# Kernel optimization log

Hardware: AMD Instinct MI355X
Metric: run time of the kernel (lower is better)

The kernel has to match this reference:

```python
import jax, jax.numpy as jnp
import numpy as np


def setup_inputs() -> dict:
    key = jax.random.key(0)
    k1, k2 = jax.random.split(key)
    B, Tc, Tq, D = 8, 2048, 1024, 1024
    similarity = jax.random.normal(k1, (B, Tc, Tq), dtype=jnp.float32)
    qencode = jax.random.normal(k2, (B, Tq, D), dtype=jnp.float32)
    return {"similarity": similarity, "qencode": qencode}


def reference(similarity, qencode):
    # softmax over query axis, then weighted sum of query encodings:
    # equivalent to softmax(similarity, -1) @ qencode, avoiding the
    # [B, Tc, Tq, D] broadcasted intermediate of the original TF code.
    attn = jax.nn.softmax(similarity, axis=-1)          # [B, Tc, Tq]
    c2q = jnp.einsum("bcq,bqd->bcd", attn, qencode)     # [B, Tc, D]
    return c2q
```

## Files before the change

kernel.cpp:

```cpp
#include <hip/hip_runtime.h>
#include <hip/hip_bf16.h>
#include <stdint.h>

#define BATCH 8
#define TC 2048
#define TQ 1024
#define DD 1024

typedef __attribute__((ext_vector_type(8))) __bf16 bf16x8;
typedef __attribute__((ext_vector_type(4))) float f32x4;

__device__ __forceinline__ ushort f2bf(float f) {
    uint32_t u = __float_as_uint(f);
    uint32_t r = (u + 0x7fffu + ((u >> 16) & 1u)) >> 16;
    return (ushort)r;
}

__global__ __launch_bounds__(256) void softmax_rows(const float* __restrict__ sim,
                                                    ushort* __restrict__ attn) {
    const int row = blockIdx.x;
    const int t = threadIdx.x;
    const int w = t >> 6, lane = t & 63;
    const float4 x = ((const float4*)(sim + (size_t)row * TQ))[t];

    float m = fmaxf(fmaxf(x.x, x.y), fmaxf(x.z, x.w));
    #pragma unroll
    for (int o = 32; o >= 1; o >>= 1) m = fmaxf(m, __shfl_xor(m, o));

    __shared__ float smax[4];
    __shared__ float ssum[4];
    if (lane == 0) smax[w] = m;
    __syncthreads();
    m = fmaxf(fmaxf(smax[0], smax[1]), fmaxf(smax[2], smax[3]));

    const float L2E = 1.4426950408889634f;
    float e0 = exp2f((x.x - m) * L2E);
    float e1 = exp2f((x.y - m) * L2E);
    float e2 = exp2f((x.z - m) * L2E);
    float e3 = exp2f((x.w - m) * L2E);

    float s = (e0 + e1) + (e2 + e3);
    #pragma unroll
    for (int o = 32; o >= 1; o >>= 1) s += __shfl_xor(s, o);
    if (lane == 0) ssum[w] = s;
    __syncthreads();
    s = (ssum[0] + ssum[1]) + (ssum[2] + ssum[3]);
    const float inv = 1.0f / s;

    ushort4 o4;
    o4.x = f2bf(e0 * inv);
    o4.y = f2bf(e1 * inv);
    o4.z = f2bf(e2 * inv);
    o4.w = f2bf(e3 * inv);
    ((ushort4*)(attn + (size_t)row * TQ))[t] = o4;
}

__global__ __launch_bounds__(256) void transpose_cast(const float* __restrict__ q,
                                                      ushort* __restrict__ qt) {
    __shared__ float tile[32][33];
    const int b = blockIdx.z;
    const int q0 = blockIdx.y * 32;
    const int d0 = blockIdx.x * 32;
    const int t = threadIdx.x;
    const int r = t >> 3;
    const int c = (t & 7) * 4;

    float4 v = *(const float4*)(q + ((size_t)b * TQ + q0 + r) * DD + d0 + c);
    tile[r][c + 0] = v.x;
    tile[r][c + 1] = v.y;
    tile[r][c + 2] = v.z;
    tile[r][c + 3] = v.w;
    __syncthreads();

    const int d = t >> 3;
    const int qq = (t & 7) * 4;
    ushort4 o4;
    o4.x = f2bf(tile[qq + 0][d]);
    o4.y = f2bf(tile[qq + 1][d]);
    o4.z = f2bf(tile[qq + 2][d]);
    o4.w = f2bf(tile[qq + 3][d]);
    *(ushort4*)(qt + ((size_t)b * DD + d0 + d) * TQ + q0 + qq) = o4;
}

__global__ __launch_bounds__(256, 2) void gemm_bf16(const ushort* __restrict__ A,
                                                    const ushort* __restrict__ Bt,
                                                    float* __restrict__ C) {
    __shared__ __align__(16) ushort As[128 * 32];
    __shared__ __align__(16) ushort Bs[128 * 32];

    const int b = blockIdx.z;
    const int tn0 = blockIdx.x * 128;
    const int tm0 = blockIdx.y * 128;
    const ushort* Ab = A + (size_t)b * TC * TQ;
    const ushort* Bb = Bt + (size_t)b * DD * TQ;
    float* Cb = C + (size_t)b * TC * DD;

    const int t = threadIdx.x;
    const int w = t >> 6, lane = t & 63;
    const int quad = lane >> 4, l16 = lane & 15;
    const int wm = (w >> 1) * 64, wn = (w & 1) * 64;

    f32x4 acc[4][4];
    #pragma unroll
    for (int i = 0; i < 4; i++)
        #pragma unroll
        for (int j = 0; j < 4; j++) acc[i][j] = (f32x4){0.f, 0.f, 0.f, 0.f};

    const int srow = w * 16 + (lane >> 2);
    const int sk = (lane & 3) * 8;

    for (int kk = 0; kk < TQ; kk += 32) {
        #pragma unroll
        for (int j = 0; j < 2; j++) {
            const ushort* ga = Ab + (size_t)(tm0 + j * 64 + srow) * TQ + kk + sk;
            const ushort* gb = Bb + (size_t)(tn0 + j * 64 + srow) * TQ + kk + sk;
            char* la = (char*)As + j * 4096 + w * 1024;
            char* lb = (char*)Bs + j * 4096 + w * 1024;
            __builtin_amdgcn_global_load_lds(
                (const __attribute__((address_space(1))) void*)ga,
                (__attribute__((address_space(3))) void*)la, 16, 0, 0);
            __builtin_amdgcn_global_load_lds(
                (const __attribute__((address_space(1))) void*)gb,
                (__attribute__((address_space(3))) void*)lb, 16, 0, 0);
        }
        __syncthreads();

        bf16x8 af[4], bfr[4];
        #pragma unroll
        for (int mi = 0; mi < 4; mi++)
            af[mi] = *(const bf16x8*)&As[(wm + mi * 16 + l16) * 32 + quad * 8];
        #pragma unroll
        for (int ni = 0; ni < 4; ni++)
            bfr[ni] = *(const bf16x8*)&Bs[(wn + ni * 16 + l16) * 32 + quad * 8];

        #pragma unroll
        for (int mi = 0; mi < 4; mi++)
            #pragma unroll
            for (int ni = 0; ni < 4; ni++)
                acc[mi][ni] = __builtin_amdgcn_mfma_f32_16x16x32_bf16(
                    af[mi], bfr[ni], acc[mi][ni], 0, 0, 0);
        __syncthreads();
    }

    #pragma unroll
    for (int mi = 0; mi < 4; mi++) {
        const int r0 = tm0 + wm + mi * 16 + quad * 4;
        #pragma unroll
        for (int ni = 0; ni < 4; ni++) {
            const int c = tn0 + wn + ni * 16 + l16;
            f32x4 v = acc[mi][ni];
            #pragma unroll
            for (int r = 0; r < 4; r++) Cb[(size_t)(r0 + r) * DD + c] = v[r];
        }
    }
}

extern "C" void kernel_launch(void* const* d_in, const int* in_sizes, int n_in,
                              void* d_out, int out_size, void* d_ws, size_t ws_size,
                              hipStream_t stream) {
    const float* sim = (const float*)d_in[0];
    const float* qen = (const float*)d_in[1];
    float* out = (float*)d_out;

    ushort* attn = (ushort*)d_ws;
    ushort* qt = (ushort*)d_ws + (size_t)BATCH * TC * TQ;

    softmax_rows<<<BATCH * TC, 256, 0, stream>>>(sim, attn);
    transpose_cast<<<dim3(DD / 32, TQ / 32, BATCH), 256, 0, stream>>>(qen, qt);
    gemm_bf16<<<dim3(DD / 128, TC / 128, BATCH), 256, 0, stream>>>(attn, qt, out);
}
```

Baseline: 192.5 us.

## Use one wave per softmax row, larger transpose tiles, grouped GEMM tile order

Softmax now handles one row per wavefront, with four rows per block. This removes the shared-memory reductions and block barriers. The transpose-cast kernel moves to 64x64 tiles so each block does more work and fewer blocks are launched. The GEMM grid becomes a flat 1D launch with grouped tile ordering, so neighbouring blocks share A and B tiles in L2. The remap assumes fixed dimensions (128 tiles per batch), and the 64x65 LDS tile raises shared memory use per transpose block.

```diff
diff --git a/kernel.cpp b/kernel.cpp
--- a/kernel.cpp
+++ b/kernel.cpp
@@ -18,68 +18,80 @@
 
 __global__ __launch_bounds__(256) void softmax_rows(const float* __restrict__ sim,
                                                     ushort* __restrict__ attn) {
-    const int row = blockIdx.x;
-    const int t = threadIdx.x;
-    const int w = t >> 6, lane = t & 63;
-    const float4 x = ((const float4*)(sim + (size_t)row * TQ))[t];
+    const int wid = threadIdx.x >> 6;
+    const int lane = threadIdx.x & 63;
+    const int row = blockIdx.x * 4 + wid;
+    const float4* src = (const float4*)(sim + (size_t)row * TQ);
 
-    float m = fmaxf(fmaxf(x.x, x.y), fmaxf(x.z, x.w));
+    float4 x[4];
+    #pragma unroll
+    for (int j = 0; j < 4; j++) x[j] = src[lane + 64 * j];
+
+    float m = -INFINITY;
+    #pragma unroll
+    for (int j = 0; j < 4; j++)
+        m = fmaxf(m, fmaxf(fmaxf(x[j].x, x[j].y), fmaxf(x[j].z, x[j].w)));
     #pragma unroll
     for (int o = 32; o >= 1; o >>= 1) m = fmaxf(m, __shfl_xor(m, o));
 
-    __shared__ float smax[4];
-    __shared__ float ssum[4];
-    if (lane == 0) smax[w] = m;
-    __syncthreads();
-    m = fmaxf(fmaxf(smax[0], smax[1]), fmaxf(smax[2], smax[3]));
-
     const float L2E = 1.4426950408889634f;
-    float e0 = exp2f((x.x - m) * L2E);
-    float e1 = exp2f((x.y - m) * L2E);
-    float e2 = exp2f((x.z - m) * L2E);
-    float e3 = exp2f((x.w - m) * L2E);
-
-    float s = (e0 + e1) + (e2 + e3);
+    float e[4][4];
+    float s = 0.f;
+    #pragma unroll
+    for (int j = 0; j < 4; j++) {
+        e[j][0] = exp2f((x[j].x - m) * L2E);
+        e[j][1] = exp2f((x[j].y - m) * L2E);
+        e[j][2] = exp2f((x[j].z - m) * L2E);
+        e[j][3] = exp2f((x[j].w - m) * L2E);
+        s += (e[j][0] + e[j][1]) + (e[j][2] + e[j][3]);
+    }
     #pragma unroll
     for (int o = 32; o >= 1; o >>= 1) s += __shfl_xor(s, o);
-    if (lane == 0) ssum[w] = s;
-    __syncthreads();
-    s = (ssum[0] + ssum[1]) + (ssum[2] + ssum[3]);
     const float inv = 1.0f / s;
 
-    ushort4 o4;
-    o4.x = f2bf(e0 * inv);
-    o4.y = f2bf(e1 * inv);
-    o4.z = f2bf(e2 * inv);
-    o4.w = f2bf(e3 * inv);
-    ((ushort4*)(attn + (size_t)row * TQ))[t] = o4;
+    ushort4* dst = (ushort4*)(attn + (size_t)row * TQ);
+    #pragma unroll
+    for (int j = 0; j < 4; j++) {
+        ushort4 o4;
+        o4.x = f2bf(e[j][0] * inv);
+        o4.y = f2bf(e[j][1] * inv);
+        o4.z = f2bf(e[j][2] * inv);
+        o4.w = f2bf(e[j][3] * inv);
+        dst[lane + 64 * j] = o4;
+    }
 }
 
 __global__ __launch_bounds__(256) void transpose_cast(const float* __restrict__ q,
                                                       ushort* __restrict__ qt) {
-    __shared__ float tile[32][33];
+    __shared__ float tile[64][65];
     const int b = blockIdx.z;
-    const int q0 = blockIdx.y * 32;
-    const int d0 = blockIdx.x * 32;
+    const int q0 = blockIdx.y * 64;
+    const int d0 = blockIdx.x * 64;
     const int t = threadIdx.x;
-    const int r = t >> 3;
-    const int c = (t & 7) * 4;
+    const int r = t >> 4;
+    const int c = (t & 15) * 4;
 
-    float4 v = *(const float4*)(q + ((size_t)b * TQ + q0 + r) * DD + d0 + c);
-    tile[r][c + 0] = v.x;
-    tile[r][c + 1] = v.y;
-    tile[r][c + 2] = v.z;
-    tile[r][c + 3] = v.w;
+    #pragma unroll
+    for (int it = 0; it < 4; it++) {
+        float4 v = *(const float4*)(q + ((size_t)b * TQ + q0 + r + it * 16) * DD + d0 + c);
+        tile[r + it * 16][c + 0] = v.x;
+        tile[r + it * 16][c + 1] = v.y;
+        tile[r + it * 16][c + 2] = v.z;
+        tile[r + it * 16][c + 3] = v.w;
+    }
     __syncthreads();
 
-    const int d = t >> 3;
-    const int qq = (t & 7) * 4;
-    ushort4 o4;
-    o4.x = f2bf(tile[qq + 0][d]);
-    o4.y = f2bf(tile[qq + 1][d]);
-    o4.z = f2bf(tile[qq + 2][d]);
-    o4.w = f2bf(tile[qq + 3][d]);
-    *(ushort4*)(qt + ((size_t)b * DD + d0 + d) * TQ + q0 + qq) = o4;
+    #pragma unroll
+    for (int it = 0; it < 4; it++) {
+        const int d = (t >> 4) + it * 16;
+        const int qq = (t & 15) * 4;
+        ushort4 o4;
+        o4.x = f2bf(tile[qq + 0][d]);
+        o4.y = f2bf(tile[qq + 1][d]);
+        o4.z = f2bf(tile[qq + 2][d]);
+        o4.w = f2bf(tile[qq + 3][d]);
+        *(ushort4*)(qt + ((size_t)b * DD + d0 + d) * TQ + q0 + qq) = o4;
+    }
 }
 
 __global__ __launch_bounds__(256, 2) void gemm_bf16(const ushort* __restrict__ A,
@@ -88,9 +100,15 @@
     __shared__ __align__(16) ushort As[128 * 32];
     __shared__ __align__(16) ushort Bs[128 * 32];
 
-    const int b = blockIdx.z;
-    const int tn0 = blockIdx.x * 128;
-    const int tm0 = blockIdx.y * 128;
+    const int flat = blockIdx.x;
+    const int b = flat >> 7;
+    const int rem = flat & 127;
+    const int group = rem >> 5;
+    const int mi_t = group * 4 + (rem & 3);
+    const int ni_t = (rem >> 2) & 7;
+    const int tm0 = mi_t * 128;
+    const int tn0 = ni_t * 128;
+
     const ushort* Ab = A + (size_t)b * TC * TQ;
     const ushort* Bb = Bt + (size_t)b * DD * TQ;
     float* Cb = C + (size_t)b * TC * DD;
@@ -165,7 +183,7 @@
     ushort* attn = (ushort*)d_ws;
     ushort* qt = (ushort*)d_ws + (size_t)BATCH * TC * TQ;
 
-    softmax_rows<<<BATCH * TC, 256, 0, stream>>>(sim, attn);
-    transpose_cast<<<dim3(DD / 32, TQ / 32, BATCH), 256, 0, stream>>>(qen, qt);
-    gemm_bf16<<<dim3(DD / 128, TC / 128, BATCH), 256, 0, stream>>>(attn, qt, out);
+    softmax_rows<<<BATCH * TC / 4, 256, 0, stream>>>(sim, attn);
+    transpose_cast<<<dim3(DD / 64, TQ / 64, BATCH), 256, 0, stream>>>(qen, qt);
+    gemm_bf16<<<BATCH * (TC / 128) * (DD / 128), 256, 0, stream>>>(attn, qt, out);
 }
```

New measurement: 186.2 us. 3.3% less time.
